# Kernel optimization log

Measured on AMD Instinct MI355X. Metric: run time of the kernel, lower is better.

Reference implementation:

```python
import jax, jax.numpy as jnp
import numpy as np

EPS = 1e-05

def setup_inputs() -> dict:
    key = jax.random.key(0)
    inputs = jax.random.normal(key, (32, 512, 768), dtype=jnp.float32)
    return {"inputs": inputs}

def reference(inputs) -> jnp.ndarray:
    # position weight: L2 norm per token, w[b,l] = sqrt(1e-5 + sum_d x^2)
    w = jnp.sqrt(EPS + jnp.sum(inputs * inputs, axis=-1))  # [B, L]
    # output[b,d,e] = sum_l w[b,l] * x[b,l,d] * x[b,l,e]
    # fused weighted Gram matrix; never materializes [B,L,D,D]
    return jnp.einsum('bld,ble->bde', inputs * w[..., None], inputs)
```

## Files before the change

kernel.cpp:

```cpp
#include <hip/hip_runtime.h>
#include <hip/hip_bf16.h>

#define BATCH 32
#define LL 512
#define DD 768
#define EPSC 1e-5f

typedef __attribute__((ext_vector_type(8))) short bf16x8;
typedef __attribute__((ext_vector_type(4))) float f32x4;

__global__ __launch_bounds__(256) void k_scales(const float* __restrict__ x,
                                                float* __restrict__ s) {
    int wave = threadIdx.x >> 6;
    int lane = threadIdx.x & 63;
    int row = blockIdx.x * 4 + wave;
    const float4* xr = (const float4*)(x + (size_t)row * DD);
    float sum = 0.f;
#pragma unroll
    for (int i = 0; i < 3; i++) {
        float4 v = xr[lane + i * 64];
        sum += v.x * v.x + v.y * v.y + v.z * v.z + v.w * v.w;
    }
#pragma unroll
    for (int off = 32; off > 0; off >>= 1)
        sum += __shfl_xor(sum, off, 64);
    if (lane == 0) s[row] = sqrtf(sqrtf(EPSC + sum));
}

__global__ __launch_bounds__(256) void k_transpose(const float* __restrict__ x,
                                                   const float* __restrict__ s,
                                                   ushort* __restrict__ yt) {
    __shared__ float tile[64][65];
    __shared__ float svec[64];
    int b = blockIdx.z;
    int l0 = blockIdx.y * 64;
    int d0 = blockIdx.x * 64;
    int t = threadIdx.x;
    if (t < 64) svec[t] = s[b * LL + l0 + t];
    const float* xp = x + ((size_t)b * LL + l0) * DD + d0;
    int f = t & 15, lr0 = t >> 4;
#pragma unroll
    for (int r = 0; r < 4; r++) {
        int l = lr0 + r * 16;
        float4 v = *(const float4*)(xp + (size_t)l * DD + f * 4);
#pragma unroll
        for (int j = 0; j < 4; j++)
            tile[l][f * 4 + j] = ((const float*)&v)[j];
    }
    __syncthreads();
    ushort* yp = yt + ((size_t)b * DD + d0) * LL + l0;
    int lc = t & 7, dl0 = t >> 3;
#pragma unroll
    for (int it = 0; it < 2; it++) {
        int d = dl0 + it * 32;
        bf16x8 w;
#pragma unroll
        for (int j = 0; j < 8; j++) {
            int l = lc * 8 + j;
            float v = tile[l][d] * svec[l];
            __hip_bfloat16 h = __float2bfloat16(v);
            w[j] = *(short*)&h;
        }
        *(bf16x8*)(yp + (size_t)d * LL + lc * 8) = w;
    }
}

__global__ __launch_bounds__(64) void k_gemm(const ushort* __restrict__ yt,
                                             float* __restrict__ out) {
    int i = blockIdx.x;
    int xcd = i & 7, slot = i >> 3;
    int b = xcd + 8 * (slot / 78);
    int p = slot % 78;
    int t = p, tm = 0, rem = 12;
    while (t >= rem) { t -= rem; rem--; tm++; }
    int tn = tm + t;
    bool diag = (tm == tn);
    int m0 = tm * 64, n0 = tn * 64;
    int lane = threadIdx.x;
    int fr = lane & 15, ks4 = lane >> 4;
    const ushort* yb = yt + (size_t)b * DD * LL;
    const ushort* pa = yb + (size_t)(m0 + fr) * LL + ks4 * 8;
    const ushort* pb = yb + (size_t)(n0 + fr) * LL + ks4 * 8;
    if (diag) pb = pa;

    f32x4 acc[4][4];
#pragma unroll
    for (int ii = 0; ii < 4; ii++)
#pragma unroll
        for (int j = 0; j < 4; j++) acc[ii][j] = (f32x4){0.f, 0.f, 0.f, 0.f};

#pragma unroll 2
    for (int ks = 0; ks < 16; ks++) {
        bf16x8 af[4], bg[4];
#pragma unroll
        for (int ii = 0; ii < 4; ii++)
            af[ii] = *(const bf16x8*)(pa + (size_t)ii * 16 * LL + ks * 32);
#pragma unroll
        for (int j = 0; j < 4; j++)
            bg[j] = *(const bf16x8*)(pb + (size_t)j * 16 * LL + ks * 32);
#pragma unroll
        for (int ii = 0; ii < 4; ii++)
#pragma unroll
            for (int j = 0; j < 4; j++)
                acc[ii][j] = __builtin_amdgcn_mfma_f32_16x16x32_bf16(
                    af[ii], bg[j], acc[ii][j], 0, 0, 0);
    }

    float* op = out + (size_t)b * DD * DD;
#pragma unroll
    for (int ii = 0; ii < 4; ii++) {
        int colb = m0 + ii * 16 + ks4 * 4;
#pragma unroll
        for (int j = 0; j < 4; j++) {
            int row = n0 + j * 16 + fr;
            float4 v = {acc[ii][j][0], acc[ii][j][1], acc[ii][j][2], acc[ii][j][3]};
            *(float4*)(op + (size_t)row * DD + colb) = v;
        }
    }
    if (!diag) {
#pragma unroll
        for (int ii = 0; ii < 4; ii++) {
            int mbase = m0 + ii * 16 + ks4 * 4;
#pragma unroll
            for (int j = 0; j < 4; j++) {
                int n = n0 + j * 16 + fr;
#pragma unroll
                for (int r = 0; r < 4; r++)
                    op[(size_t)(mbase + r) * DD + n] = acc[ii][j][r];
            }
        }
    }
}

extern "C" void kernel_launch(void* const* d_in, const int* in_sizes, int n_in,
                              void* d_out, int out_size, void* d_ws, size_t ws_size,
                              hipStream_t stream) {
    const float* x = (const float*)d_in[0];
    float* s = (float*)d_ws;
    ushort* yt = (ushort*)((char*)d_ws + 65536);

    k_scales<<<dim3((BATCH * LL) / 4), 256, 0, stream>>>(x, s);
    k_transpose<<<dim3(DD / 64, LL / 64, BATCH), 256, 0, stream>>>(x, s, yt);
    k_gemm<<<dim3(78 * BATCH), 64, 0, stream>>>(yt, (float*)d_out);
}
```

Measured before the change: 159.0 us.

## Split GEMM K dimension across four waves with LDS reduction

Each GEMM block grows from one wave to four. Each wave handles a quarter of the K=512 reduction, and the partial accumulators are combined through a two-stage shared-memory tree reduction. The two surviving waves then each write half the output tile. The aim is more latency-hiding parallelism per tile and a shorter serial MFMA chain, paid for with LDS traffic, three barriers and extra shared memory per block.

```diff
diff --git a/kernel.cpp b/kernel.cpp
--- a/kernel.cpp
+++ b/kernel.cpp
@@ -65,8 +65,9 @@
     }
 }
 
-__global__ __launch_bounds__(64) void k_gemm(const ushort* __restrict__ yt,
-                                             float* __restrict__ out) {
+__global__ __launch_bounds__(256) void k_gemm(const ushort* __restrict__ yt,
+                                              float* __restrict__ out) {
+    __shared__ f32x4 red[2][16][64];
     int i = blockIdx.x;
     int xcd = i & 7, slot = i >> 3;
     int b = xcd + 8 * (slot / 78);
@@ -76,7 +77,8 @@
     int tn = tm + t;
     bool diag = (tm == tn);
     int m0 = tm * 64, n0 = tn * 64;
-    int lane = threadIdx.x;
+    int tid = threadIdx.x;
+    int wv = tid >> 6, lane = tid & 63;
     int fr = lane & 15, ks4 = lane >> 4;
     const ushort* yb = yt + (size_t)b * DD * LL;
     const ushort* pa = yb + (size_t)(m0 + fr) * LL + ks4 * 8;
@@ -89,15 +91,16 @@
 #pragma unroll
         for (int j = 0; j < 4; j++) acc[ii][j] = (f32x4){0.f, 0.f, 0.f, 0.f};
 
-#pragma unroll 2
-    for (int ks = 0; ks < 16; ks++) {
+#pragma unroll
+    for (int ksl = 0; ksl < 4; ksl++) {
+        int ko = (wv * 4 + ksl) * 32;
         bf16x8 af[4], bg[4];
 #pragma unroll
         for (int ii = 0; ii < 4; ii++)
-            af[ii] = *(const bf16x8*)(pa + (size_t)ii * 16 * LL + ks * 32);
+            af[ii] = *(const bf16x8*)(pa + (size_t)ii * 16 * LL + ko);
 #pragma unroll
         for (int j = 0; j < 4; j++)
-            bg[j] = *(const bf16x8*)(pb + (size_t)j * 16 * LL + ks * 32);
+            bg[j] = *(const bf16x8*)(pb + (size_t)j * 16 * LL + ko);
 #pragma unroll
         for (int ii = 0; ii < 4; ii++)
 #pragma unroll
@@ -106,20 +109,56 @@
                     af[ii], bg[j], acc[ii][j], 0, 0, 0);
     }
 
+    if (wv >= 2) {
+#pragma unroll
+        for (int ii = 0; ii < 4; ii++)
+#pragma unroll
+            for (int j = 0; j < 4; j++)
+                red[wv - 2][ii * 4 + j][lane] = acc[ii][j];
+    }
+    __syncthreads();
+    if (wv < 2) {
+#pragma unroll
+        for (int ii = 0; ii < 4; ii++)
+#pragma unroll
+            for (int j = 0; j < 4; j++)
+                acc[ii][j] += red[wv][ii * 4 + j][lane];
+    }
+    __syncthreads();
+    if (wv < 2) {
+        int base = (wv == 0) ? 2 : 0;
+#pragma unroll
+        for (int i2 = 0; i2 < 2; i2++)
+#pragma unroll
+            for (int j = 0; j < 4; j++)
+                red[wv][i2 * 4 + j][lane] = acc[base + i2][j];
+    }
+    __syncthreads();
+    if (wv >= 2) return;
+    int iiLo = (wv == 0) ? 0 : 2;
+#pragma unroll
+    for (int i2 = 0; i2 < 2; i2++)
+#pragma unroll
+        for (int j = 0; j < 4; j++)
+            acc[iiLo + i2][j] += red[wv ^ 1][i2 * 4 + j][lane];
+
     float* op = out + (size_t)b * DD * DD;
 #pragma unroll
-    for (int ii = 0; ii < 4; ii++) {
+    for (int i2 = 0; i2 < 2; i2++) {
+        int ii = iiLo + i2;
         int colb = m0 + ii * 16 + ks4 * 4;
 #pragma unroll
         for (int j = 0; j < 4; j++) {
             int row = n0 + j * 16 + fr;
-            float4 v = {acc[ii][j][0], acc[ii][j][1], acc[ii][j][2], acc[ii][j][3]};
+            f32x4 a = acc[ii][j];
+            float4 v = {a[0], a[1], a[2], a[3]};
             *(float4*)(op + (size_t)row * DD + colb) = v;
         }
     }
     if (!diag) {
 #pragma unroll
-        for (int ii = 0; ii < 4; ii++) {
+        for (int i2 = 0; i2 < 2; i2++) {
+            int ii = iiLo + i2;
             int mbase = m0 + ii * 16 + ks4 * 4;
 #pragma unroll
             for (int j = 0; j < 4; j++) {
@@ -141,5 +180,5 @@
 
     k_scales<<<dim3((BATCH * LL) / 4), 256, 0, stream>>>(x, s);
     k_transpose<<<dim3(DD / 64, LL / 64, BATCH), 256, 0, stream>>>(x, s, yt);
-    k_gemm<<<dim3(78 * BATCH), 64, 0, stream>>>(yt, (float*)d_out);
+    k_gemm<<<dim3(78 * BATCH), 256, 0, stream>>>(yt, (float*)d_out);
 }
```

After: 270.0 us. +69.8%, slower.
